# Performance work log

Measured on AMD Instinct MI355X. Metric: run time of the kernel, lower is better.

## Reference

```python
import jax, jax.numpy as jnp
import numpy as np

INIT_DIM = 512
HID = 1024
OUT = 64
N_NODES = 100000
N_NBR = 65536


def setup_inputs() -> dict:
    key = jax.random.key(0)
    ks = jax.random.split(key, 12)
    inp = {}
    inp["feat"] = jax.random.normal(ks[0], (1, INIT_DIM), dtype=jnp.float32)
    for i, t in enumerate("abc"):
        inp[f"all_feat_{t}"] = jax.random.normal(ks[1 + i], (N_NODES, INIT_DIM), dtype=jnp.float32)
        inp[f"nbr_{t}"] = jax.random.randint(ks[4 + i], (N_NBR,), 0, N_NODES)
        inp[f"W1_{t}"] = jax.random.normal(ks[7 + i], (HID, INIT_DIM), dtype=jnp.float32) * 0.02
        inp[f"b1_{t}"] = jnp.zeros((HID,), dtype=jnp.float32)
    inp["Wc"] = jax.random.normal(ks[10], (OUT, HID), dtype=jnp.float32) * 0.02
    inp["bc"] = jnp.zeros((OUT,), dtype=jnp.float32)
    return inp


def reference(feat, all_feat_a, all_feat_b, all_feat_c,
              nbr_a, nbr_b, nbr_c,
              W1_a, b1_a, W1_b, b1_b, W1_c, b1_c, Wc, bc):
    # trans1 = 'rel-linear': per-type neighbor gather + relation-specific Linear
    # h_j: [N_NBR, HID]
    h_a = all_feat_a[nbr_a] @ W1_a.T + b1_a
    h_b = all_feat_b[nbr_b] @ W1_b.T + b1_b
    h_c = all_feat_c[nbr_c] @ W1_c.T + b1_c
    # trans2 = 'none' (passthrough); concat aggregation over all types
    h = jnp.concatenate([h_a, h_b, h_c], axis=0)  # [3*N_NBR, HID]
    h = jax.nn.relu(h)                             # activate = 'relu'
    pooled = h.mean(axis=0)                        # agg_node = 'mean' -> [HID]
    feat_all = jax.nn.relu(pooled)
    logits = feat_all @ Wc.T + bc                  # [OUT]
    return logits
```

## Files before the change

### kernel.cpp

```cpp
#include <hip/hip_runtime.h>
#include <hip/hip_bf16.h>

typedef __attribute__((ext_vector_type(4))) float f32x4;
typedef __attribute__((ext_vector_type(4))) int   int4v;
typedef __attribute__((ext_vector_type(2))) int   int2v;
typedef __attribute__((ext_vector_type(16))) int  i32x16;

#define N_NBR 65536
#define INIT_DIM 512
#define HID 1024
#define NTILE 3072
#define NBLOCK 512
#define TPB 6
#define SA 24.0f
#define SW 1024.0f
#define INVS (1.0f / (24.0f * 1024.0f))

static __device__ __forceinline__ int q8(float x, float s) {
  float y = fminf(fmaxf(x * s, -127.f), 127.f);
  return __float2int_rn(y);
}
static __device__ __forceinline__ int pack4(float a, float b, float c, float d, float s) {
  return (q8(a,s) & 255) | ((q8(b,s) & 255) << 8) | ((q8(c,s) & 255) << 16) | ((q8(d,s) & 255) << 24);
}

__global__ __launch_bounds__(256) void k_convw(const float* __restrict__ wa,
                                               const float* __restrict__ wb,
                                               const float* __restrict__ wc,
                                               char* __restrict__ out) {
  int g = blockIdx.x * 256 + threadIdx.x;
  int l = g & 63;
  int blk = g >> 6;
  int ks = blk & 15;
  int nb = (blk >> 4) & 31;
  int t = blk >> 9;
  const float* src = (t == 0) ? wa : (t == 1) ? wb : wc;
  int n = nb * 32 + (l & 31);
  int k0 = ks * 32 + (l >> 5) * 16;
  const f32x4* p = (const f32x4*)(src + (size_t)n * INIT_DIM + k0);
  f32x4 x0 = p[0], x1 = p[1], x2 = p[2], x3 = p[3];
  int4v v;
  v[0] = pack4(x0.x, x0.y, x0.z, x0.w, SW);
  v[1] = pack4(x1.x, x1.y, x1.z, x1.w, SW);
  v[2] = pack4(x2.x, x2.y, x2.z, x2.w, SW);
  v[3] = pack4(x3.x, x3.y, x3.z, x3.w, SW);
  *(int4v*)(out + (size_t)g * 16) = v;
}

__global__ __launch_bounds__(256) void k_main(
    const float* __restrict__ fa, const float* __restrict__ fb, const float* __restrict__ fc,
    const int* __restrict__ na, const int* __restrict__ nb_, const int* __restrict__ nc__,
    const float* __restrict__ b1a, const float* __restrict__ b1b, const float* __restrict__ b1c,
    const char* __restrict__ wbf8,
    float* __restrict__ partials) {
  __shared__ __align__(16) char Asm[2][64 * 512];

  int bx = blockIdx.x;
  int tid = threadIdx.x;
  int wave = tid >> 6;
  int lane = tid & 63;
  int l31 = lane & 31, hi = lane >> 5;

  auto featsel = [&](int t) { return (t == 0) ? fa : (t == 1) ? fb : fc; };
  auto nbrsel  = [&](int t) { return (t == 0) ? na : (t == 1) ? nb_ : nc__; };
  auto biassel = [&](int t) { return (t == 0) ? b1a : (t == 1) ? b1b : b1c; };

  unsigned swz = (unsigned)l31 << 4;
  unsigned abase = (unsigned)l31 * 512u + (((unsigned)hi << 4) ^ (swz & 16u));
  unsigned swzhi = swz & 0x1E0u;

  int tile0 = bx * TPB;
  int idxr[16];
  f32x4 hold[4][2];

  {
    int t0 = tile0 >> 10, mt0 = tile0 & 1023;
    const int* nbr0 = nbrsel(t0);
    const float* feat0 = featsel(t0);
    #pragma unroll 2
    for (int c = 0; c < 16; ++c) {
      int r = c * 4 + wave;
      int idx = nbr0[mt0 * 64 + r];
      const float* rp = feat0 + (size_t)idx * INIT_DIM + lane * 8;
      f32x4 a  = *(const f32x4*)rp;
      f32x4 b2 = *((const f32x4*)rp + 1);
      int2v v;
      v[0] = pack4(a.x, a.y, a.z, a.w, SA);
      v[1] = pack4(b2.x, b2.y, b2.z, b2.w, SA);
      unsigned byte = (unsigned)r * 512u +
                      (((unsigned)lane * 8u) ^ ((unsigned)(r & 31) << 4));
      *(int2v*)(&Asm[0][0] + byte) = v;
    }
    int tn = tile0 + 1;
    const int* nbr1 = nbrsel(tn >> 10);
    int mt1 = tn & 1023;
    #pragma unroll
    for (int c = 0; c < 16; ++c) idxr[c] = nbr1[mt1 * 64 + c * 4 + wave];
  }
  __syncthreads();

  for (int q = 0; q < TPB; ++q) {
    int tile_id = tile0 + q;
    int t = tile_id >> 10;
    const char* Wf8 = wbf8 + (size_t)t * (32 * 16 * 1024);
    const float* bias = biassel(t);
    const char* rbuf = &Asm[q & 1][0];
    char* wbuf = &Asm[(q + 1) & 1][0];
    bool pf = (q + 1 < TPB);
    const float* featn = pf ? featsel((tile_id + 1) >> 10) : fa;

    #pragma unroll
    for (int p = 0; p < 4; ++p) {
      if (pf) {
        #pragma unroll
        for (int k = 0; k < 4; ++k) {
          int idx = idxr[p * 4 + k];
          const float* rp = featn + (size_t)idx * INIT_DIM + lane * 8;
          hold[k][0] = *(const f32x4*)rp;
          hold[k][1] = *((const f32x4*)rp + 1);
        }
      }
      const char* pBa = Wf8 + ((size_t)(wave * 8 + p * 2)     << 14) + lane * 16;
      const char* pBb = Wf8 + ((size_t)(wave * 8 + p * 2 + 1) << 14) + lane * 16;
      i32x16 acc[2] = {};
      i32x16 acd[2] = {};
      #pragma unroll 4
      for (int ks = 0; ks < 16; ++ks) {
        int4v Bf0 = *(const int4v*)(pBa + (ks << 10));
        int4v Bf1 = *(const int4v*)(pBb + (ks << 10));
        unsigned kcol = (((unsigned)ks << 5) ^ swzhi);
        int4v Af0 = *(const int4v*)(rbuf + (abase + kcol));
        int4v Af1 = *(const int4v*)(rbuf + (abase + 16384u + kcol));
        acc[0] = __builtin_amdgcn_mfma_i32_32x32x32_i8(Af0, Bf0, acc[0], 0, 0, 0);
        acc[1] = __builtin_amdgcn_mfma_i32_32x32x32_i8(Af0, Bf1, acc[1], 0, 0, 0);
        acd[0] = __builtin_amdgcn_mfma_i32_32x32x32_i8(Af1, Bf0, acd[0], 0, 0, 0);
        acd[1] = __builtin_amdgcn_mfma_i32_32x32x32_i8(Af1, Bf1, acd[1], 0, 0, 0);
      }
      #pragma unroll
      for (int j = 0; j < 2; ++j) {
        int n = (wave * 8 + p * 2 + j) * 32 + l31;
        int bq = __float2int_rn(bias[n] * (SA * SW));
        int s = 0;
        #pragma unroll
        for (int r = 0; r < 16; ++r) s += max(acc[j][r] + bq, 0);
        #pragma unroll
        for (int r = 0; r < 16; ++r) s += max(acd[j][r] + bq, 0);
        s += __shfl_xor(s, 32);
        if (hi == 0) partials[(size_t)tile_id * HID + n] = (float)s * INVS;
      }
      if (pf) {
        #pragma unroll
        for (int k = 0; k < 4; ++k) {
          int r = (p * 4 + k) * 4 + wave;
          f32x4 a = hold[k][0], b2 = hold[k][1];
          int2v v;
          v[0] = pack4(a.x, a.y, a.z, a.w, SA);
          v[1] = pack4(b2.x, b2.y, b2.z, b2.w, SA);
          unsigned byte = (unsigned)r * 512u +
                          (((unsigned)lane * 8u) ^ ((unsigned)(r & 31) << 4));
          *(int2v*)(wbuf + byte) = v;
        }
      }
    }
    if (pf && q + 2 < TPB) {
      int tn2 = tile_id + 2;
      const int* nbrn = nbrsel(tn2 >> 10);
      int mtn = tn2 & 1023;
      #pragma unroll
      for (int c = 0; c < 16; ++c) idxr[c] = nbrn[mtn * 64 + c * 4 + wave];
    }
    __syncthreads();
  }
}

__global__ __launch_bounds__(256) void k_reduce1(const float* __restrict__ partials,
                                                 float* __restrict__ inter) {
  int b = blockIdx.x;
  int tid = threadIdx.x;
  const f32x4* base = (const f32x4*)(partials + (size_t)b * 16 * HID) + tid;
  f32x4 s = {0.f, 0.f, 0.f, 0.f};
  #pragma unroll 4
  for (int r = 0; r < 16; ++r) {
    f32x4 v = base[r * (HID / 4)];
    s.x += v.x; s.y += v.y; s.z += v.z; s.w += v.w;
  }
  *((f32x4*)(inter + (size_t)b * HID) + tid) = s;
}

__global__ __launch_bounds__(1024) void k_reduce2(const float* __restrict__ inter,
                                                  float* __restrict__ acc) {
  int col = threadIdx.x;
  float s = 0.f;
  #pragma unroll 8
  for (int r = 0; r < 192; ++r) s += inter[(size_t)r * HID + col];
  acc[col] = s;
}

__global__ __launch_bounds__(256) void k_final(const float* __restrict__ acc,
                                               const float* __restrict__ Wc,
                                               const float* __restrict__ bc,
                                               float* __restrict__ out) {
  __shared__ float fall[HID];
  int tid = threadIdx.x;
  const float inv = 1.f / (3.f * (float)N_NBR);
  for (int i = tid; i < HID; i += 256) {
    float p = acc[i] * inv;
    fall[i] = (p > 0.f) ? p : 0.f;
  }
  __syncthreads();
  int o = tid >> 2, q = tid & 3;
  const f32x4* w = (const f32x4*)(Wc + (size_t)o * HID + q * 256);
  const f32x4* f = (const f32x4*)(fall + q * 256);
  float s = 0.f;
  #pragma unroll 4
  for (int k = 0; k < 64; ++k) {
    f32x4 wv = w[k], fv = f[k];
    s += wv.x * fv.x + wv.y * fv.y + wv.z * fv.z + wv.w * fv.w;
  }
  s += __shfl_xor(s, 1);
  s += __shfl_xor(s, 2);
  if (q == 0) out[o] = s + bc[o];
}

extern "C" void kernel_launch(void* const* d_in, const int* in_sizes, int n_in,
                              void* d_out, int out_size, void* d_ws, size_t ws_size,
                              hipStream_t stream) {
  const float* fa  = (const float*)d_in[1];
  const int*   na  = (const int*)d_in[2];
  const float* W1a = (const float*)d_in[3];
  const float* b1a = (const float*)d_in[4];
  const float* fb  = (const float*)d_in[5];
  const int*   nb  = (const int*)d_in[6];
  const float* W1b = (const float*)d_in[7];
  const float* b1b = (const float*)d_in[8];
  const float* fc  = (const float*)d_in[9];
  const int*   nc  = (const int*)d_in[10];
  const float* W1c = (const float*)d_in[11];
  const float* b1c = (const float*)d_in[12];
  const float* Wc  = (const float*)d_in[13];
  const float* bc  = (const float*)d_in[14];
  float* out = (float*)d_out;

  float* acc = (float*)d_ws;
  char*  wbf8 = (char*)d_ws + 4096;
  float* partials = (float*)((char*)d_ws + 4096 + 3 * 32 * 16 * 1024);
  float* inter = partials + (size_t)NTILE * HID;

  k_convw<<<384, 256, 0, stream>>>(W1a, W1b, W1c, wbf8);
  k_main<<<NBLOCK, 256, 0, stream>>>(fa, fb, fc, na, nb, nc, b1a, b1b, b1c, wbf8, partials);
  k_reduce1<<<192, 256, 0, stream>>>(partials, inter);
  k_reduce2<<<1, 1024, 0, stream>>>(inter, acc);
  k_final<<<1, 256, 0, stream>>>(acc, Wc, bc, out);
}
```

Before: 178.7 us.

## Specialize waves into gather/quantize producers and MFMA consumers

After: 285.7 us. +59.9%, slower.

```diff
diff --git a/kernel.cpp b/kernel.cpp
--- a/kernel.cpp
+++ b/kernel.cpp
@@ -65,13 +65,7 @@
   auto nbrsel  = [&](int t) { return (t == 0) ? na : (t == 1) ? nb_ : nc__; };
   auto biassel = [&](int t) { return (t == 0) ? b1a : (t == 1) ? b1b : b1c; };
 
-  unsigned swz = (unsigned)l31 << 4;
-  unsigned abase = (unsigned)l31 * 512u + (((unsigned)hi << 4) ^ (swz & 16u));
-  unsigned swzhi = swz & 0x1E0u;
-
   int tile0 = bx * TPB;
-  int idxr[16];
-  f32x4 hold[4][2];
 
   {
     int t0 = tile0 >> 10, mt0 = tile0 & 1023;
@@ -91,68 +85,31 @@
                       (((unsigned)lane * 8u) ^ ((unsigned)(r & 31) << 4));
       *(int2v*)(&Asm[0][0] + byte) = v;
     }
-    int tn = tile0 + 1;
-    const int* nbr1 = nbrsel(tn >> 10);
-    int mt1 = tn & 1023;
-    #pragma unroll
-    for (int c = 0; c < 16; ++c) idxr[c] = nbr1[mt1 * 64 + c * 4 + wave];
   }
   __syncthreads();
+
+  unsigned swz = (unsigned)l31 << 4;
+  unsigned abase = (unsigned)l31 * 512u + (((unsigned)hi << 4) ^ (swz & 16u));
+  unsigned swzhi = swz & 0x1E0u;
 
   for (int q = 0; q < TPB; ++q) {
     int tile_id = tile0 + q;
     int t = tile_id >> 10;
-    const char* Wf8 = wbf8 + (size_t)t * (32 * 16 * 1024);
-    const float* bias = biassel(t);
-    const char* rbuf = &Asm[q & 1][0];
-    char* wbuf = &Asm[(q + 1) & 1][0];
-    bool pf = (q + 1 < TPB);
-    const float* featn = pf ? featsel((tile_id + 1) >> 10) : fa;
-
-    #pragma unroll
-    for (int p = 0; p < 4; ++p) {
-      if (pf) {
-        #pragma unroll
-        for (int k = 0; k < 4; ++k) {
-          int idx = idxr[p * 4 + k];
+
+    if (wave < 2) {
+      if (q + 1 < TPB) {
+        int tn = tile_id + 1;
+        int tt = tn >> 10, mtn = tn & 1023;
+        const int* nbrn = nbrsel(tt);
+        const float* featn = featsel(tt);
+        char* wbuf = &Asm[(q + 1) & 1][0];
+        #pragma unroll 4
+        for (int c = 0; c < 32; ++c) {
+          int r = c * 2 + wave;
+          int idx = nbrn[mtn * 64 + r];
           const float* rp = featn + (size_t)idx * INIT_DIM + lane * 8;
-          hold[k][0] = *(const f32x4*)rp;
-          hold[k][1] = *((const f32x4*)rp + 1);
-        }
-      }
-      const char* pBa = Wf8 + ((size_t)(wave * 8 + p * 2)     << 14) + lane * 16;
-      const char* pBb = Wf8 + ((size_t)(wave * 8 + p * 2 + 1) << 14) + lane * 16;
-      i32x16 acc[2] = {};
-      i32x16 acd[2] = {};
-      #pragma unroll 4
-      for (int ks = 0; ks < 16; ++ks) {
-        int4v Bf0 = *(const int4v*)(pBa + (ks << 10));
-        int4v Bf1 = *(const int4v*)(pBb + (ks << 10));
-        unsigned kcol = (((unsigned)ks << 5) ^ swzhi);
-        int4v Af0 = *(const int4v*)(rbuf + (abase + kcol));
-        int4v Af1 = *(const int4v*)(rbuf + (abase + 16384u + kcol));
-        acc[0] = __builtin_amdgcn_mfma_i32_32x32x32_i8(Af0, Bf0, acc[0], 0, 0, 0);
-        acc[1] = __builtin_amdgcn_mfma_i32_32x32x32_i8(Af0, Bf1, acc[1], 0, 0, 0);
-        acd[0] = __builtin_amdgcn_mfma_i32_32x32x32_i8(Af1, Bf0, acd[0], 0, 0, 0);
-        acd[1] = __builtin_amdgcn_mfma_i32_32x32x32_i8(Af1, Bf1, acd[1], 0, 0, 0);
-      }
-      #pragma unroll
-      for (int j = 0; j < 2; ++j) {
-        int n = (wave * 8 + p * 2 + j) * 32 + l31;
-        int bq = __float2int_rn(bias[n] * (SA * SW));
-        int s = 0;
-        #pragma unroll
-        for (int r = 0; r < 16; ++r) s += max(acc[j][r] + bq, 0);
-        #pragma unroll
-        for (int r = 0; r < 16; ++r) s += max(acd[j][r] + bq, 0);
-        s += __shfl_xor(s, 32);
-        if (hi == 0) partials[(size_t)tile_id * HID + n] = (float)s * INVS;
-      }
-      if (pf) {
-        #pragma unroll
-        for (int k = 0; k < 4; ++k) {
-          int r = (p * 4 + k) * 4 + wave;
-          f32x4 a = hold[k][0], b2 = hold[k][1];
+          f32x4 a  = *(const f32x4*)rp;
+          f32x4 b2 = *((const f32x4*)rp + 1);
           int2v v;
           v[0] = pack4(a.x, a.y, a.z, a.w, SA);
           v[1] = pack4(b2.x, b2.y, b2.z, b2.w, SA);
@@ -161,13 +118,45 @@
           *(int2v*)(wbuf + byte) = v;
         }
       }
-    }
-    if (pf && q + 2 < TPB) {
-      int tn2 = tile_id + 2;
-      const int* nbrn = nbrsel(tn2 >> 10);
-      int mtn = tn2 & 1023;
-      #pragma unroll
-      for (int c = 0; c < 16; ++c) idxr[c] = nbrn[mtn * 64 + c * 4 + wave];
+    } else {
+      int cw = wave - 2;
+      const char* rbuf = &Asm[q & 1][0];
+      const char* Wf8 = wbf8 + (size_t)t * (32 * 16 * 1024);
+      const float* bias = biassel(t);
+      #pragma unroll 2
+      for (int p = 0; p < 8; ++p) {
+        const char* pBa = Wf8 + ((size_t)(cw * 16 + p * 2)     << 14) + lane * 16;
+        const char* pBb = Wf8 + ((size_t)(cw * 16 + p * 2 + 1) << 14) + lane * 16;
+        i32x16 acc[2][2] = {};
+        #pragma unroll 4
+        for (int ks = 0; ks < 16; ++ks) {
+          int4v Bf0 = *(const int4v*)(pBa + (ks << 10));
+          int4v Bf1 = *(const int4v*)(pBb + (ks << 10));
+          unsigned kcol = (((unsigned)ks << 5) ^ swzhi);
+          int4v Af[2];
+          #pragma unroll
+          for (int i = 0; i < 2; ++i)
+            Af[i] = *(const int4v*)(rbuf + (abase + (unsigned)(i * 16384) + kcol));
+          #pragma unroll
+          for (int i = 0; i < 2; ++i) {
+            acc[i][0] = __builtin_amdgcn_mfma_i32_32x32x32_i8(Af[i], Bf0, acc[i][0], 0, 0, 0);
+            acc[i][1] = __builtin_amdgcn_mfma_i32_32x32x32_i8(Af[i], Bf1, acc[i][1], 0, 0, 0);
+          }
+        }
+        #pragma unroll
+        for (int j = 0; j < 2; ++j) {
+          int n = (cw * 16 + p * 2 + j) * 32 + l31;
+          int bq = __float2int_rn(bias[n] * (SA * SW));
+          int s = 0;
+          #pragma unroll
+          for (int i = 0; i < 2; ++i)
+            #pragma unroll
+            for (int r = 0; r < 16; ++r)
+              s += max(acc[i][j][r] + bq, 0);
+          s += __shfl_xor(s, 32);
+          if (hi == 0) partials[(size_t)tile_id * HID + n] = (float)s * INVS;
+        }
+      }
     }
     __syncthreads();
   }
```
